# Performance work log

Hardware: AMD Instinct MI355X
Metric: run time of the kernel (lower is better)

Reference implementation:

```python
import jax, jax.numpy as jnp
import numpy as np

K = 3          # k_neighbors
EPS = 1e-12    # F.normalize eps


def _l2norm(x):
    n = jnp.sqrt(jnp.sum(x * x, axis=-1, keepdims=True))
    return x / jnp.maximum(n, EPS)


def setup_inputs() -> dict:
    key = jax.random.key(0)
    k1, k2 = jax.random.split(key)
    query_features = jax.random.normal(k1, (64, 64, 32, 32), dtype=jnp.float32)
    support_features = jax.random.normal(k2, (64, 5, 64, 1024), dtype=jnp.float32)
    return {"query_features": query_features, "support_features": support_features}


def reference(query_features, support_features):
    B, D, h, w = query_features.shape
    # (B, Nq, D), L2-normalized along D
    q_local = _l2norm(query_features.reshape(B, D, h * w).transpose(0, 2, 1))
    # support: (B, Way, D, Ns) -> (B, Way, Ns, D), L2-normalized along D
    s_local = _l2norm(support_features.transpose(0, 1, 3, 2))
    # cosine similarities for all (batch, way) pairs in one batched matmul
    sim = jnp.einsum('bqd,bwsd->bwqs', q_local, s_local)  # (B, Way, Nq, Ns)
    k_actual = min(K, sim.shape[-1])
    topk_sim, _ = jax.lax.top_k(sim, k_actual)            # (B, Way, Nq, k)
    return topk_sim.sum(axis=(-1, -2))                    # (B, Way)
```

## Files before the change

kernel.cpp:

```cpp
#include <hip/hip_runtime.h>
#include <hip/hip_bf16.h>


using bf16x8 = __attribute__((ext_vector_type(8))) short;
using f32x4  = __attribute__((ext_vector_type(4))) float;

__device__ inline unsigned cvt_pk_bf16(float lo, float hi) {
    unsigned r;
    asm("v_cvt_pk_bf16_f32 %0, %1, %2" : "=v"(r) : "v"(lo), "v"(hi));
    return r;
}

__device__ inline uint4 pack8cvt(const float* v) {
    uint4 r;
    r.x = cvt_pk_bf16(v[0], v[1]);
    r.y = cvt_pk_bf16(v[2], v[3]);
    r.z = cvt_pk_bf16(v[4], v[5]);
    r.w = cvt_pk_bf16(v[6], v[7]);
    return r;
}

#define INS(v, T0, T1, T2) do {                         \
    float _v = (v);                                     \
    float _n0 = fmaxf((T0), _v);                        \
    float _n1 = __builtin_amdgcn_fmed3f(_v, (T0), (T1));\
    float _n2 = __builtin_amdgcn_fmed3f(_v, (T1), (T2));\
    (T0) = _n0; (T1) = _n1; (T2) = _n2;                 \
} while (0)


__global__ __launch_bounds__(256) void prep_q(const float* __restrict__ Q,
                                              uint4* __restrict__ Qbf,
                                              float* __restrict__ rnq) {
    const int b = blockIdx.x >> 2;
    const int col = ((blockIdx.x & 3) << 8) + threadIdx.x;
    const float* p = Q + (size_t)b * 65536 + col;
    float v[64];
    #pragma unroll
    for (int d = 0; d < 64; ++d) v[d] = p[(size_t)d << 10];
    float ss = 0.f;
    #pragma unroll
    for (int d = 0; d < 64; ++d) ss += v[d] * v[d];
    rnq[(b << 10) + col] = 1.0f / fmaxf(sqrtf(ss), 1e-12f);
    uint4* ob = Qbf + ((size_t)(b << 6) + (col >> 4)) * 128 + (col & 15);
    #pragma unroll
    for (int h = 0; h < 8; ++h)
        ob[h << 4] = pack8cvt(&v[h << 3]);
}

__global__ __launch_bounds__(256) void prep_s(const float* __restrict__ S,
                                              uint4* __restrict__ Sbf) {
    const int bw = blockIdx.x >> 2;
    const int col = ((blockIdx.x & 3) << 8) + threadIdx.x;
    const float* p = S + (size_t)bw * 65536 + col;
    float v[64];
    #pragma unroll
    for (int d = 0; d < 64; ++d) v[d] = p[(size_t)d << 10];
    float ss = 0.f;
    #pragma unroll
    for (int d = 0; d < 64; ++d) ss += v[d] * v[d];
    const float rs = 1.0f / fmaxf(sqrtf(ss), 1e-12f);
    #pragma unroll
    for (int d = 0; d < 64; ++d) v[d] *= rs;
    uint4* ob = Sbf + ((size_t)(bw << 6) + (col >> 4)) * 128 + (col & 15);
    #pragma unroll
    for (int h = 0; h < 8; ++h)
        ob[h << 4] = pack8cvt(&v[h << 3]);
}

__global__ __launch_bounds__(256) void knn_main(const uint4* __restrict__ Qbf,
                                                const uint4* __restrict__ Sbf,
                                                const float* __restrict__ rnq,
                                                float* __restrict__ partial) {
    __shared__ float wsum[4];
    const int qc = blockIdx.x, w = blockIdx.y, b = blockIdx.z;
    const int wv = threadIdx.x >> 6, lane = threadIdx.x & 63;

    const uint4* qb = Qbf + ((size_t)(b << 6) + (qc << 4) + (wv << 2)) * 128 + lane;
    bf16x8 bq[4][2];
    #pragma unroll
    for (int qt = 0; qt < 4; ++qt)
        #pragma unroll
        for (int c = 0; c < 2; ++c)
            bq[qt][c] = *reinterpret_cast<const bf16x8*>(&qb[qt * 128 + (c << 6)]);

    const uint4* sb = Sbf + (size_t)((b * 5 + w) << 6) * 128 + lane;

    float t0[4], t1[4], t2[4];
    #pragma unroll
    for (int qt = 0; qt < 4; ++qt) { t0[qt] = -1e30f; t1[qt] = -1e30f; t2[qt] = -1e30f; }

    bf16x8 a0 = *reinterpret_cast<const bf16x8*>(&sb[0]);
    bf16x8 a1 = *reinterpret_cast<const bf16x8*>(&sb[64]);
    #pragma unroll 4
    for (int st = 0; st < 64; ++st) {
        const bf16x8 c0 = a0, c1 = a1;
        if (st < 63) {
            a0 = *reinterpret_cast<const bf16x8*>(&sb[(st + 1) * 128]);
            a1 = *reinterpret_cast<const bf16x8*>(&sb[(st + 1) * 128 + 64]);
        }
        #pragma unroll
        for (int qt = 0; qt < 4; ++qt) {
            f32x4 c = {0.f, 0.f, 0.f, 0.f};
            c = __builtin_amdgcn_mfma_f32_16x16x32_bf16(c0, bq[qt][0], c, 0, 0, 0);
            c = __builtin_amdgcn_mfma_f32_16x16x32_bf16(c1, bq[qt][1], c, 0, 0, 0);
            #pragma unroll
            for (int j = 0; j < 4; ++j)
                INS(c[j], t0[qt], t1[qt], t2[qt]);
        }
    }

    float s3 = 0.f;
    #pragma unroll
    for (int qt = 0; qt < 4; ++qt) {
        #pragma unroll
        for (int m = 16; m <= 32; m <<= 1) {
            float b0 = __shfl_xor(t0[qt], m);
            float b1 = __shfl_xor(t1[qt], m);
            float b2 = __shfl_xor(t2[qt], m);
            INS(b0, t0[qt], t1[qt], t2[qt]);
            INS(b1, t0[qt], t1[qt], t2[qt]);
            INS(b2, t0[qt], t1[qt], t2[qt]);
        }
        const int qg = (qc << 8) + (wv << 6) + (qt << 4) + (lane & 15);
        s3 += (t0[qt] + t1[qt] + t2[qt]) * rnq[(b << 10) + qg];
    }
    #pragma unroll
    for (int m = 1; m < 64; m <<= 1) s3 += __shfl_xor(s3, m);
    s3 *= 0.25f;
    if (lane == 0) wsum[wv] = s3;
    __syncthreads();
    if (threadIdx.x == 0)
        partial[((b * 5 + w) << 2) + qc] = (wsum[0] + wsum[1]) + (wsum[2] + wsum[3]);
}

__global__ void finalize4(const float* __restrict__ partial, float* __restrict__ out) {
    int i = blockIdx.x * blockDim.x + threadIdx.x;
    if (i < 320)
        out[i] = (partial[4 * i] + partial[4 * i + 1]) +
                 (partial[4 * i + 2] + partial[4 * i + 3]);
}

__global__ void norms_kernel(const float* __restrict__ Q, const float* __restrict__ S,
                             float* __restrict__ rnq, float* __restrict__ rns) {
    int gid = blockIdx.x * blockDim.x + threadIdx.x;
    if (gid < 65536) {
        int b = gid >> 10, qi = gid & 1023;
        const float* p = Q + (size_t)b * 65536 + qi;
        float ss = 0.f;
        #pragma unroll
        for (int d = 0; d < 64; ++d) { float v = p[(size_t)d * 1024]; ss += v * v; }
        rnq[gid] = 1.0f / fmaxf(sqrtf(ss), 1e-12f);
    } else {
        int v = gid - 65536;
        int bw = v >> 10, si = v & 1023;
        const float* p = S + (size_t)bw * 65536 + si;
        float ss = 0.f;
        #pragma unroll
        for (int d = 0; d < 64; ++d) { float x = p[(size_t)d * 1024]; ss += x * x; }
        rns[v] = 1.0f / fmaxf(sqrtf(ss), 1e-12f);
    }
}

__global__ __launch_bounds__(512, 4) void knn_fb(
        const float* __restrict__ Q, const float* __restrict__ S,
        const float* __restrict__ rnq, const float* __restrict__ rns,
        float* __restrict__ partial) {
    __shared__ uint4 qfrag[16 * 128];
    __shared__ uint4 sfrag[2][4 * 128];
    __shared__ float wsum[8];

    const int qc = blockIdx.x, w = blockIdx.y, b = blockIdx.z;
    const int t = threadIdx.x, wv = t >> 6, lane = t & 63;

    const float* Qb   = Q + (size_t)b * 65536;
    const float* Sb   = S + (size_t)(b * 5 + w) * 65536;
    const float* rnqb = rnq + (b << 10);
    const float* rnsb = rns + ((b * 5 + w) << 10);

    bf16x8 bq[4][2];
    for (int ph = 0; ph < 2; ++ph) {
        for (int sub = 0; sub < 4; ++sub) {
            int qg = (qc << 9) + (ph << 8) + (sub << 6) + lane;
            float v[8];
            #pragma unroll
            for (int i = 0; i < 8; ++i)
                v[i] = Qb[(size_t)((wv << 3) + i) * 1024 + qg];
            qfrag[((sub << 2) + (lane >> 4)) * 128 + (wv << 4) + (lane & 15)] = pack8cvt(v);
        }
        __syncthreads();
        if ((wv >> 2) == ph) {
            #pragma unroll
            for (int qt = 0; qt < 4; ++qt)
                #pragma unroll
                for (int c = 0; c < 2; ++c)
                    bq[qt][c] = *reinterpret_cast<const bf16x8*>(
                        &qfrag[(((wv & 3) << 2) + qt) * 128 + (c << 6) + lane]);
        }
        __syncthreads();
    }

    {
        float sv[8]; float rs = rnsb[lane];
        #pragma unroll
        for (int i = 0; i < 8; ++i)
            sv[i] = Sb[(size_t)((wv << 3) + i) * 1024 + lane] * rs;
        sfrag[0][(lane >> 4) * 128 + (wv << 4) + (lane & 15)] = pack8cvt(sv);
    }
    __syncthreads();

    float t0[4], t1[4], t2[4];
    #pragma unroll
    for (int qt = 0; qt < 4; ++qt) { t0[qt] = -1e30f; t1[qt] = -1e30f; t2[qt] = -1e30f; }
    int cur = 0;
    const float* sp = Sb + ((wv << 3) << 10) + lane;

    for (int blk = 0; blk < 16; ++blk) {
        float sv[8]; float rs;
        if (blk < 15) {
            const int sb_ = (blk + 1) << 6;
            rs = rnsb[sb_ + lane];
            #pragma unroll
            for (int i = 0; i < 8; ++i)
                sv[i] = sp[(size_t)(i << 10) + sb_];
        }
        #pragma unroll
        for (int st = 0; st < 4; ++st) {
            bf16x8 a0 = *reinterpret_cast<const bf16x8*>(&sfrag[cur][st * 128 + lane]);
            bf16x8 a1 = *reinterpret_cast<const bf16x8*>(&sfrag[cur][st * 128 + 64 + lane]);
            #pragma unroll
            for (int qt = 0; qt < 4; ++qt) {
                f32x4 c = {0.f, 0.f, 0.f, 0.f};
                c = __builtin_amdgcn_mfma_f32_16x16x32_bf16(a0, bq[qt][0], c, 0, 0, 0);
                c = __builtin_amdgcn_mfma_f32_16x16x32_bf16(a1, bq[qt][1], c, 0, 0, 0);
                #pragma unroll
                for (int j = 0; j < 4; ++j)
                    INS(c[j], t0[qt], t1[qt], t2[qt]);
            }
        }
        if (blk < 15) {
            #pragma unroll
            for (int i = 0; i < 8; ++i) sv[i] *= rs;
            sfrag[cur ^ 1][(lane >> 4) * 128 + (wv << 4) + (lane & 15)] = pack8cvt(sv);
        }
        __syncthreads();
        cur ^= 1;
    }

    float s3 = 0.f;
    #pragma unroll
    for (int qt = 0; qt < 4; ++qt) {
        #pragma unroll
        for (int m = 16; m <= 32; m <<= 1) {
            float b0 = __shfl_xor(t0[qt], m);
            float b1 = __shfl_xor(t1[qt], m);
            float b2 = __shfl_xor(t2[qt], m);
            INS(b0, t0[qt], t1[qt], t2[qt]);
            INS(b1, t0[qt], t1[qt], t2[qt]);
            INS(b2, t0[qt], t1[qt], t2[qt]);
        }
        int qg = (qc << 9) + (wv << 6) + (qt << 4) + (lane & 15);
        s3 += (t0[qt] + t1[qt] + t2[qt]) * rnqb[qg];
    }
    #pragma unroll
    for (int m = 1; m < 64; m <<= 1) s3 += __shfl_xor(s3, m);
    s3 *= 0.25f;
    if (lane == 0) wsum[wv] = s3;
    __syncthreads();
    if (t == 0) {
        float acc = 0.f;
        #pragma unroll
        for (int i = 0; i < 8; ++i) acc += wsum[i];
        partial[((b * 5 + w) << 1) + qc] = acc;
    }
}

__global__ void finalize2(const float* __restrict__ partial, float* __restrict__ out) {
    int i = blockIdx.x * blockDim.x + threadIdx.x;
    if (i < 320)
        out[i] = partial[2 * i] + partial[2 * i + 1];
}

extern "C" void kernel_launch(void* const* d_in, const int* in_sizes, int n_in,
                              void* d_out, int out_size, void* d_ws, size_t ws_size,
                              hipStream_t stream) {
    const float* Q = (const float*)d_in[0];
    const float* S = (const float*)d_in[1];
    float* out = (float*)d_out;

    const size_t NEED = 8388608ull + 41943040ull + 262144ull + 5120ull;
    if (ws_size >= NEED) {
        uint4* Qbf    = (uint4*)d_ws;
        uint4* Sbf    = (uint4*)((char*)d_ws + 8388608ull);
        float* rnq    = (float*)((char*)d_ws + 8388608ull + 41943040ull);
        float* partial= (float*)((char*)d_ws + 8388608ull + 41943040ull + 262144ull);
        prep_q<<<256, 256, 0, stream>>>(Q, Qbf, rnq);
        prep_s<<<1280, 256, 0, stream>>>(S, Sbf);
        knn_main<<<dim3(4, 5, 64), 256, 0, stream>>>(Qbf, Sbf, rnq, partial);
        finalize4<<<2, 256, 0, stream>>>(partial, out);
    } else {
        float* rnq = (float*)d_ws;
        float* rns = rnq + 65536;
        float* partial = rns + 327680;
        norms_kernel<<<(65536 + 327680) / 256, 256, 0, stream>>>(Q, S, rnq, rns);
        knn_fb<<<dim3(2, 5, 64), 512, 0, stream>>>(Q, S, rnq, rns, partial);
        finalize2<<<2, 256, 0, stream>>>(partial, out);
    }
}
```

Measured before the change: 99.54 us.

## Merge prep kernels, remap knn blocks across XCDs, deepen support prefetch

Merges the query and support preprocessing into one launch, which removes a kernel launch and the gap between the two prep kernels. The knn_main grid is flattened and block indices are remapped ((lin&7)*160 + lin>>3). This is presumably meant to place the blocks that share a batch on the same XCD so they share L2 for the Q tiles. The support prefetch changes from one tile ahead to a 4-slot ring buffer loading three tiles ahead, to hide more global load latency. The deeper prefetch costs extra registers, which could reduce occupancy.

```diff
diff --git a/kernel.cpp b/kernel.cpp
--- a/kernel.cpp
+++ b/kernel.cpp
@@ -29,43 +29,45 @@
 } while (0)
 
 
-__global__ __launch_bounds__(256) void prep_q(const float* __restrict__ Q,
-                                              uint4* __restrict__ Qbf,
-                                              float* __restrict__ rnq) {
-    const int b = blockIdx.x >> 2;
-    const int col = ((blockIdx.x & 3) << 8) + threadIdx.x;
-    const float* p = Q + (size_t)b * 65536 + col;
-    float v[64];
-    #pragma unroll
-    for (int d = 0; d < 64; ++d) v[d] = p[(size_t)d << 10];
-    float ss = 0.f;
-    #pragma unroll
-    for (int d = 0; d < 64; ++d) ss += v[d] * v[d];
-    rnq[(b << 10) + col] = 1.0f / fmaxf(sqrtf(ss), 1e-12f);
-    uint4* ob = Qbf + ((size_t)(b << 6) + (col >> 4)) * 128 + (col & 15);
-    #pragma unroll
-    for (int h = 0; h < 8; ++h)
-        ob[h << 4] = pack8cvt(&v[h << 3]);
-}
-
-__global__ __launch_bounds__(256) void prep_s(const float* __restrict__ S,
-                                              uint4* __restrict__ Sbf) {
-    const int bw = blockIdx.x >> 2;
-    const int col = ((blockIdx.x & 3) << 8) + threadIdx.x;
-    const float* p = S + (size_t)bw * 65536 + col;
-    float v[64];
-    #pragma unroll
-    for (int d = 0; d < 64; ++d) v[d] = p[(size_t)d << 10];
-    float ss = 0.f;
-    #pragma unroll
-    for (int d = 0; d < 64; ++d) ss += v[d] * v[d];
-    const float rs = 1.0f / fmaxf(sqrtf(ss), 1e-12f);
-    #pragma unroll
-    for (int d = 0; d < 64; ++d) v[d] *= rs;
-    uint4* ob = Sbf + ((size_t)(bw << 6) + (col >> 4)) * 128 + (col & 15);
-    #pragma unroll
-    for (int h = 0; h < 8; ++h)
-        ob[h << 4] = pack8cvt(&v[h << 3]);
+__global__ __launch_bounds__(256) void prep_all(const float* __restrict__ Q,
+                                                const float* __restrict__ S,
+                                                uint4* __restrict__ Qbf,
+                                                uint4* __restrict__ Sbf,
+                                                float* __restrict__ rnq) {
+    const int blk = blockIdx.x;
+    if (blk < 256) {
+        const int b = blk >> 2;
+        const int col = ((blk & 3) << 8) + threadIdx.x;
+        const float* p = Q + (size_t)b * 65536 + col;
+        float v[64];
+        #pragma unroll
+        for (int d = 0; d < 64; ++d) v[d] = p[(size_t)d << 10];
+        float ss = 0.f;
+        #pragma unroll
+        for (int d = 0; d < 64; ++d) ss += v[d] * v[d];
+        rnq[(b << 10) + col] = 1.0f / fmaxf(sqrtf(ss), 1e-12f);
+        uint4* ob = Qbf + ((size_t)(b << 6) + (col >> 4)) * 128 + (col & 15);
+        #pragma unroll
+        for (int h = 0; h < 8; ++h)
+            ob[h << 4] = pack8cvt(&v[h << 3]);
+    } else {
+        const int bw = (blk - 256) >> 2;
+        const int col = ((blk & 3) << 8) + threadIdx.x;
+        const float* p = S + (size_t)bw * 65536 + col;
+        float v[64];
+        #pragma unroll
+        for (int d = 0; d < 64; ++d) v[d] = p[(size_t)d << 10];
+        float ss = 0.f;
+        #pragma unroll
+        for (int d = 0; d < 64; ++d) ss += v[d] * v[d];
+        const float rs = 1.0f / fmaxf(sqrtf(ss), 1e-12f);
+        #pragma unroll
+        for (int d = 0; d < 64; ++d) v[d] *= rs;
+        uint4* ob = Sbf + ((size_t)(bw << 6) + (col >> 4)) * 128 + (col & 15);
+        #pragma unroll
+        for (int h = 0; h < 8; ++h)
+            ob[h << 4] = pack8cvt(&v[h << 3]);
+    }
 }
 
 __global__ __launch_bounds__(256) void knn_main(const uint4* __restrict__ Qbf,
@@ -73,7 +75,11 @@
                                                 const float* __restrict__ rnq,
                                                 float* __restrict__ partial) {
     __shared__ float wsum[4];
-    const int qc = blockIdx.x, w = blockIdx.y, b = blockIdx.z;
+    const int lin = blockIdx.x;
+    const int l   = (lin & 7) * 160 + (lin >> 3);
+    const int qc  = l & 3;
+    const int bw  = l >> 2;
+    const int b   = bw / 5;
     const int wv = threadIdx.x >> 6, lane = threadIdx.x & 63;
 
     const uint4* qb = Qbf + ((size_t)(b << 6) + (qc << 4) + (wv << 2)) * 128 + lane;
@@ -84,26 +90,29 @@
         for (int c = 0; c < 2; ++c)
             bq[qt][c] = *reinterpret_cast<const bf16x8*>(&qb[qt * 128 + (c << 6)]);
 
-    const uint4* sb = Sbf + (size_t)((b * 5 + w) << 6) * 128 + lane;
+    const uint4* sb = Sbf + (size_t)(bw << 6) * 128 + lane;
 
     float t0[4], t1[4], t2[4];
     #pragma unroll
     for (int qt = 0; qt < 4; ++qt) { t0[qt] = -1e30f; t1[qt] = -1e30f; t2[qt] = -1e30f; }
 
-    bf16x8 a0 = *reinterpret_cast<const bf16x8*>(&sb[0]);
-    bf16x8 a1 = *reinterpret_cast<const bf16x8*>(&sb[64]);
+    bf16x8 abuf[4][2];
+    #pragma unroll
+    for (int i = 0; i < 3; ++i) {
+        abuf[i][0] = *reinterpret_cast<const bf16x8*>(&sb[i * 128]);
+        abuf[i][1] = *reinterpret_cast<const bf16x8*>(&sb[i * 128 + 64]);
+    }
     #pragma unroll 4
     for (int st = 0; st < 64; ++st) {
-        const bf16x8 c0 = a0, c1 = a1;
-        if (st < 63) {
-            a0 = *reinterpret_cast<const bf16x8*>(&sb[(st + 1) * 128]);
-            a1 = *reinterpret_cast<const bf16x8*>(&sb[(st + 1) * 128 + 64]);
+        if (st + 3 < 64) {
+            abuf[(st + 3) & 3][0] = *reinterpret_cast<const bf16x8*>(&sb[(st + 3) * 128]);
+            abuf[(st + 3) & 3][1] = *reinterpret_cast<const bf16x8*>(&sb[(st + 3) * 128 + 64]);
         }
         #pragma unroll
         for (int qt = 0; qt < 4; ++qt) {
             f32x4 c = {0.f, 0.f, 0.f, 0.f};
-            c = __builtin_amdgcn_mfma_f32_16x16x32_bf16(c0, bq[qt][0], c, 0, 0, 0);
-            c = __builtin_amdgcn_mfma_f32_16x16x32_bf16(c1, bq[qt][1], c, 0, 0, 0);
+            c = __builtin_amdgcn_mfma_f32_16x16x32_bf16(abuf[st & 3][0], bq[qt][0], c, 0, 0, 0);
+            c = __builtin_amdgcn_mfma_f32_16x16x32_bf16(abuf[st & 3][1], bq[qt][1], c, 0, 0, 0);
             #pragma unroll
             for (int j = 0; j < 4; ++j)
                 INS(c[j], t0[qt], t1[qt], t2[qt]);
@@ -131,7 +140,7 @@
     if (lane == 0) wsum[wv] = s3;
     __syncthreads();
     if (threadIdx.x == 0)
-        partial[((b * 5 + w) << 2) + qc] = (wsum[0] + wsum[1]) + (wsum[2] + wsum[3]);
+        partial[((size_t)bw << 2) + qc] = (wsum[0] + wsum[1]) + (wsum[2] + wsum[3]);
 }
 
 __global__ void finalize4(const float* __restrict__ partial, float* __restrict__ out) {
@@ -294,9 +303,8 @@
         uint4* Sbf    = (uint4*)((char*)d_ws + 8388608ull);
         float* rnq    = (float*)((char*)d_ws + 8388608ull + 41943040ull);
         float* partial= (float*)((char*)d_ws + 8388608ull + 41943040ull + 262144ull);
-        prep_q<<<256, 256, 0, stream>>>(Q, Qbf, rnq);
-        prep_s<<<1280, 256, 0, stream>>>(S, Sbf);
-        knn_main<<<dim3(4, 5, 64), 256, 0, stream>>>(Qbf, Sbf, rnq, partial);
+        prep_all<<<1536, 256, 0, stream>>>(Q, S, Qbf, Sbf, rnq);
+        knn_main<<<1280, 256, 0, stream>>>(Qbf, Sbf, rnq, partial);
         finalize4<<<2, 256, 0, stream>>>(partial, out);
     } else {
         float* rnq = (float*)d_ws;
```

After: 96.50 us. 3.1% less time.
